# Performance work log

Measured on AMD Instinct MI355X. Metric: run time of the kernel, lower is better.

The kernel has to match this reference:

```python
import jax, jax.numpy as jnp
import numpy as np

N_SPECIES = 119
N_RADIAL = 5
N_BASIS = 7
R_MIN = 0.5
R_MAX = 6.0
UNITS = (512, 512)
EMB_NORM = 1.0 / np.sqrt(N_BASIS)
N_ATOMS = 20000
N_PAIRS = 800000
N_FEAT = 360  # gaussian moments for n_radial=5, n_contr=8

# triangular index sets for symmetric contractions
_t2i, _t2j = np.tril_indices(N_RADIAL)  # 15 unique (r,s) pairs
_t3 = np.array([(i, j, k) for i in range(N_RADIAL) for j in range(i + 1) for k in range(j + 1)])
_t3i, _t3j, _t3k = _t3[:, 0], _t3[:, 1], _t3[:, 2]  # 35 unique (r,s,t) triples


def _forward(R, Z, neighbor, offsets, embeddings, W1, b1, W2, b2, W3, b3):
    n_atoms = R.shape[0]
    idx_i, idx_j = neighbor[0], neighbor[1]
    # --- distance computation (free space, init_box == 0) ---
    dr_vec = R[idx_j] - R[idx_i] + offsets                      # (P,3)
    dr = jnp.sqrt(jnp.sum(dr_vec * dr_vec, axis=-1))            # (P,)
    dn = dr_vec / (dr + 1e-5)[:, None]                          # unit vectors
    # --- gaussian radial basis + species-pair embedding + cosine cutoff ---
    shifts = jnp.linspace(R_MIN, R_MAX, N_BASIS)
    betta = N_BASIS ** 2 / R_MAX ** 2
    rad_norm = (2.0 * betta / np.pi) ** 0.75
    basis = rad_norm * jnp.exp(-betta * (dr[:, None] - shifts) ** 2)   # (P,B)
    cutoff = 0.5 * (jnp.cos(np.pi * dr / R_MAX) + 1.0) * (dr < R_MAX)
    emb = embeddings[Z[idx_j], Z[idx_i]]                               # (P,R,B)
    radial = EMB_NORM * jnp.einsum('prb,pb->pr', emb, basis) * cutoff[:, None]  # (P,R)
    # --- geometric moments, aggregated per central atom ---
    m1 = radial[:, :, None] * dn[:, None, :]                    # (P,R,3)
    m2 = m1[..., None] * dn[:, None, None, :]                   # (P,R,3,3)
    m3 = m2[..., None] * dn[:, None, None, None, :]             # (P,R,3,3,3)
    seg = lambda x: jax.ops.segment_sum(x, idx_i, num_segments=n_atoms)
    M0, M1, M2, M3 = seg(radial), seg(m1), seg(m2), seg(m3)
    # --- invariant contractions (gaussian moments) ---
    c1 = jnp.einsum('ari,asi->ars', M1, M1)[:, _t2i, _t2j]
    c2 = jnp.einsum('arij,asij->ars', M2, M2)[:, _t2i, _t2j]
    c3 = jnp.einsum('arijk,asijk->ars', M3, M3)[:, _t2i, _t2j]
    c4 = jnp.einsum('arij,asik,atjk->arst', M2, M2, M2)[:, _t3i, _t3j, _t3k]
    c5 = jnp.einsum('ari,asj,atij->arst', M1, M1, M2)[:, _t2i, _t2j].reshape(n_atoms, -1)
    c6 = jnp.einsum('arijk,asijl,atkl->arst', M3, M3, M2)[:, _t2i, _t2j].reshape(n_atoms, -1)
    c7 = jnp.einsum('arijk,asij,atk->arst', M3, M2, M1).reshape(n_atoms, -1)
    feats = jnp.concatenate([M0, c1, c2, c3, c4, c5, c6, c7], axis=-1)  # (A,360)
    # --- vmapped per-atom NTK readout MLP (swish) ---
    h = jax.nn.swish(feats @ W1 / np.sqrt(N_FEAT) + 0.1 * b1)
    h = jax.nn.swish(h @ W2 / np.sqrt(UNITS[0]) + 0.1 * b2)
    out = h @ W3 / np.sqrt(UNITS[1]) + 0.1 * b3                 # (A,1)
    # --- mask padded atoms (Z == 0) ---
    out = out * (Z > 0)[:, None]
    return out


def setup_inputs() -> dict:
    key = jax.random.key(0)
    ks = jax.random.split(key, 8)
    R = jax.random.uniform(ks[0], (N_ATOMS, 3), jnp.float32) * 12.0  # 12 A cube
    Z = jax.random.randint(ks[1], (N_ATOMS,), 0, N_SPECIES, jnp.int32)
    neighbor = jax.random.randint(ks[2], (2, N_PAIRS), 0, N_ATOMS, jnp.int32)
    # avoid degenerate self pairs (dr == 0 would NaN the unit vector grad)
    idx_i, idx_j = neighbor[0], neighbor[1]
    idx_j = jnp.where(idx_j == idx_i, (idx_j + 1) % N_ATOMS, idx_j)
    neighbor = jnp.stack([idx_i, idx_j], axis=0)
    box = jnp.zeros((3, 3), jnp.float32)
    offsets = jnp.zeros((N_PAIRS, 3), jnp.float32)
    embeddings = jax.random.normal(ks[3], (N_SPECIES, N_SPECIES, N_RADIAL, N_BASIS), jnp.float32)
    W1 = jax.random.normal(ks[4], (N_FEAT, UNITS[0]), jnp.float32)
    b1 = jnp.zeros((UNITS[0],), jnp.float32)
    W2 = jax.random.normal(ks[5], (UNITS[0], UNITS[1]), jnp.float32)
    b2 = jnp.zeros((UNITS[1],), jnp.float32)
    W3 = jax.random.normal(ks[6], (UNITS[1], 1), jnp.float32)
    b3 = jnp.zeros((1,), jnp.float32)
    return dict(R=R, Z=Z, neighbor=neighbor, box=box, offsets=offsets,
                embeddings=embeddings, W1=W1, b1=b1, W2=W2, b2=b2, W3=W3, b3=b3)


def reference(R, Z, neighbor, box, offsets, embeddings, W1, b1, W2, b2, W3, b3):
    # box is unused: init_box == 0 selects the free-space displacement fn
    return _forward(R, Z, neighbor, offsets, embeddings, W1, b1, W2, b2, W3, b3)
```

## Files before the change

### kernel.cpp

```cpp
#include <hip/hip_runtime.h>
#include <hip/hip_bf16.h>
#include <cmath>

#define NSP 119
#define UNITS 512
#define NFEAT 360
#define KP1 384
#define CAP 128

typedef __attribute__((ext_vector_type(8))) short short8;
typedef __attribute__((ext_vector_type(4))) float floatx4;

#define AS1 __attribute__((address_space(1)))
#define AS3 __attribute__((address_space(3)))

__device__ __forceinline__ void gload_lds16(const void* g, void* l) {
    __builtin_amdgcn_global_load_lds((AS1 void*)(size_t)g, (AS3 void*)l, 16, 0, 0);
}

__device__ __host__ constexpr int s2c(int i, int j) {
    return (i > j) ? i*(i+1)/2 + j : j*(j+1)/2 + i;
}
__device__ __host__ constexpr int s3c(int x, int y, int z) {
    int A = x > y ? x : y; A = A > z ? A : z;
    int C = x < y ? x : y; C = C < z ? C : z;
    int B = x + y + z - A - C;
    return A*(A+1)*(A+2)/6 + B*(B+1)/2 + C;
}

struct BasisConsts {
    float f0k;
    float kg;
    float scale;
    float c[6];
};

__global__ __launch_bounds__(256) void pair_prep_kernel(
    const float* __restrict__ R, const int* __restrict__ Z,
    const int* __restrict__ nbr, const float* __restrict__ offsets,
    const float* __restrict__ emb, int* __restrict__ counts,
    float* __restrict__ tmpRec, int npairs, BasisConsts bc,
    const float* __restrict__ W1, const float* __restrict__ W2,
    __hip_bfloat16* __restrict__ W1t, __hip_bfloat16* __restrict__ W2t,
    float* __restrict__ outbuf, const float* __restrict__ b3,
    int pgrid, int natoms)
{
    int blk = blockIdx.x;
    if (blk >= pgrid) {
        int b = blk - pgrid;
        if (b < 448) {
            __shared__ float tile[32][33];
            const float* W; __hip_bfloat16* Wt; int K, Kp, ik, in;
            if (b < 192) { W = W1; Wt = W1t; K = NFEAT; Kp = KP1; ik = b % 12; in = b / 12; }
            else { int b2 = b - 192; W = W2; Wt = W2t; K = UNITS; Kp = UNITS; ik = b2 & 15; in = b2 >> 4; }
            int tx = threadIdx.x & 31, ty = threadIdx.x >> 5;
            int n = in * 32 + tx;
            #pragma unroll
            for (int pp = 0; pp < 4; ++pp) {
                int kk = ty + pp * 8;
                int k = ik * 32 + kk;
                tile[kk][tx] = (k < K) ? W[(size_t)k * UNITS + n] : 0.f;
            }
            __syncthreads();
            #pragma unroll
            for (int pp = 0; pp < 4; ++pp) {
                int nn = ty + pp * 8;
                Wt[(size_t)(in * 32 + nn) * Kp + ik * 32 + tx] = __float2bfloat16(tile[tx][nn]);
            }
        } else {
            int idx = (b - 448) * 256 + threadIdx.x;
            if (idx < natoms)
                outbuf[idx] = (Z[idx] > 0) ? 0.1f * b3[0] : 0.f;
        }
        return;
    }

    int p = blk * 256 + threadIdx.x;
    if (p >= npairs) return;
    int i = nbr[p];
    int j = nbr[npairs + p];
    float dx = R[3*j]   - R[3*i]   + offsets[3*p];
    float dy = R[3*j+1] - R[3*i+1] + offsets[3*p+1];
    float dz = R[3*j+2] - R[3*i+2] + offsets[3*p+2];
    float dr2 = fmaf(dz, dz, fmaf(dy, dy, dx*dx));
    if (dr2 >= 36.0f) return;
    int pos = atomicAdd(&counts[i], 1);
    if (pos >= CAP) return;

    float dr  = sqrtf(dr2);
    float inv = 1.0f / (dr + 1e-5f);
    float d0  = dr - 0.5f;
    float basis[7];
    basis[0] = exp2f(bc.f0k * d0 * d0);
    float G  = exp2f(bc.kg * dr);
    float cur = basis[0];
    #pragma unroll
    for (int b = 0; b < 6; ++b) { cur *= G * bc.c[b]; basis[b+1] = cur; }
    float cut = 0.5f * (__cosf(dr * 0.52359877559829887f) + 1.0f);
    float s = bc.scale * cut;

    const float* e = emb + ((size_t)Z[j] * NSP + Z[i]) * 35;
    float ev[35];
    __builtin_memcpy(ev, e, 35 * sizeof(float));

    float rec[8];
    #pragma unroll
    for (int r = 0; r < 5; ++r) {
        float acc = 0.f;
        #pragma unroll
        for (int b = 0; b < 7; ++b) acc += ev[r*7+b] * basis[b];
        rec[r] = s * acc;
    }
    rec[5] = dx * inv; rec[6] = dy * inv; rec[7] = dz * inv;
    float4* out = (float4*)(tmpRec + ((size_t)i * CAP + pos) * 8);
    out[0] = make_float4(rec[0], rec[1], rec[2], rec[3]);
    out[1] = make_float4(rec[4], rec[5], rec[6], rec[7]);
}

#define SREC 28
__global__ __launch_bounds__(256) void moment_kernel(
    const float* __restrict__ tmpRec, const int* __restrict__ counts,
    float* __restrict__ momG, int natoms)
{
    int wv = threadIdx.x >> 6, lane = threadIdx.x & 63;
    int a = blockIdx.x * 4 + wv;
    __shared__ float stage[4][64][SREC];

    int cnt = 0;
    if (a < natoms) cnt = min(counts[a], CAP);

    int cr0, pk0;
    if (lane < 5)       { cr0 = lane;            pk0 = 0; }
    else if (lane < 20) { int c = lane - 5;      cr0 = c / 3;  pk0 = 1 + c % 3; }
    else if (lane < 50) { int c = lane - 20;     cr0 = c / 6;  pk0 = 4 + c % 6; }
    else                { int c = lane - 50;     cr0 = c / 10; pk0 = 10 + c % 10; }
    int cr1 = 0, pk1 = 0;
    if (lane < 36) { int c = 14 + lane; cr1 = c / 10; pk1 = 10 + c % 10; }

    float acc0 = 0.f, acc1 = 0.f;
    for (int base = 0; base < cnt; base += 64) {
        int m = min(64, cnt - base);
        if (lane < m) {
            const float4* pd = (const float4*)(tmpRec + ((size_t)a * CAP + base + lane) * 8);
            float4 u = pd[0], v = pd[1];
            float x = v.y, y = v.z, z = v.w;
            float s2_0 = x*x, s2_1 = y*x, s2_2 = y*y, s2_3 = z*x, s2_4 = z*y, s2_5 = z*z;
            float* st = stage[wv][lane];
            ((float4*)st)[0] = u;
            ((float4*)st)[1] = make_float4(v.x, 1.0f, x, y);
            ((float4*)st)[2] = make_float4(z, s2_0, s2_1, s2_2);
            ((float4*)st)[3] = make_float4(s2_3, s2_4, s2_5, s2_0*x);
            ((float4*)st)[4] = make_float4(s2_0*y, s2_2*x, s2_2*y, s2_0*z);
            ((float4*)st)[5] = make_float4(s2_1*z, s2_2*z, s2_5*x, s2_5*y);
            ((float4*)st)[6] = make_float4(s2_5*z, 0.f, 0.f, 0.f);
        }
        __builtin_amdgcn_wave_barrier();
        for (int q = 0; q < m; ++q) {
            const float* s = stage[wv][q];
            acc0 += s[cr0] * s[5 + pk0];
            acc1 += s[cr1] * s[5 + pk1];
        }
        __builtin_amdgcn_wave_barrier();
    }
    size_t base = (size_t)(a >> 6) * 6400 + (size_t)(a & 63);
    momG[base + (size_t)lane * 64] = acc0;
    if (lane < 36) momG[base + (size_t)(64 + lane) * 64] = acc1;
}

#define LROW 390
__global__ __launch_bounds__(256) void feat_kernel(
    const float* __restrict__ momG, __hip_bfloat16* __restrict__ feats)
{
    constexpr int cT2I[15] = {0,1,1,2,2,2,3,3,3,3,4,4,4,4,4};
    constexpr int cT2J[15] = {0,0,1,0,1,2,0,1,2,3,0,1,2,3,4};
    constexpr int cT3A[35] = {0, 1,1,1, 2,2,2,2,2,2, 3,3,3,3,3,3,3,3,3,3, 4,4,4,4,4,4,4,4,4,4,4,4,4,4,4};
    constexpr int cT3B[35] = {0, 0,1,1, 0,1,1,2,2,2, 0,1,1,2,2,2,3,3,3,3, 0,1,1,2,2,2,3,3,3,3,4,4,4,4,4};
    constexpr int cT3C[35] = {0, 0,0,1, 0,0,1,0,1,2, 0,0,1,0,1,2,0,1,2,3, 0,0,1,0,1,2,0,1,2,3,0,1,2,3,4};
    constexpr float cW2[6]  = {1.f,2.f,1.f,2.f,2.f,1.f};
    constexpr float cW3[10] = {1.f,3.f,3.f,1.f,3.f,6.f,3.f,3.f,3.f,1.f};

    __shared__ __hip_bfloat16 ldsF[64][LROW];
    int wv = threadIdx.x >> 6, lane = threadIdx.x & 63;
    const float* mg = momG + (size_t)blockIdx.x * 6400 + lane;

    #define LDM(e) mg[(e) * 64]
    #define STF(f, v) ldsF[lane][(f)] = __float2bfloat16(v)

    if (wv == 0) {
        float m3[50], m2[30];
        #pragma unroll
        for (int e = 0; e < 50; ++e) m3[e] = LDM(50 + e);
        #pragma unroll
        for (int e = 0; e < 30; ++e) m2[e] = LDM(20 + e);
        #pragma unroll
        for (int p = 0; p < 10; ++p) {
            int r = cT2I[p], s = cT2J[p];
            float B2v[9];
            #pragma unroll
            for (int z = 0; z < 3; ++z)
                #pragma unroll
                for (int w = 0; w < 3; ++w) {
                    float acc = 0.f;
                    #pragma unroll
                    for (int x = 0; x < 3; ++x)
                        #pragma unroll
                        for (int y = 0; y < 3; ++y)
                            acc += m3[r*10 + s3c(x,y,z)] * m3[s*10 + s3c(x,y,w)];
                    B2v[z*3+w] = acc;
                }
            #pragma unroll
            for (int t = 0; t < 5; ++t) {
                float acc = 0.f;
                #pragma unroll
                for (int z = 0; z < 3; ++z)
                    #pragma unroll
                    for (int w = 0; w < 3; ++w)
                        acc += B2v[z*3+w] * m2[t*6 + s2c(z,w)];
                STF(160 + p*5 + t, acc);
            }
        }
    } else if (wv == 1) {
        float m0[5], m1[15], m2[30];
        #pragma unroll
        for (int e = 0; e < 5; ++e)  m0[e] = LDM(e);
        #pragma unroll
        for (int e = 0; e < 15; ++e) m1[e] = LDM(5 + e);
        #pragma unroll
        for (int e = 0; e < 30; ++e) m2[e] = LDM(20 + e);
        #pragma unroll
        for (int r = 0; r < 5; ++r) STF(r, m0[r]);
        #pragma unroll
        for (int p = 0; p < 15; ++p) {
            int r = cT2I[p], s = cT2J[p];
            float v1 = m1[r*3]*m1[s*3] + m1[r*3+1]*m1[s*3+1] + m1[r*3+2]*m1[s*3+2];
            STF(5 + p, v1);
            float v2 = 0.f;
            #pragma unroll
            for (int k = 0; k < 6; ++k) v2 += cW2[k] * m2[r*6+k] * m2[s*6+k];
            STF(20 + p, v2);
        }
        #pragma unroll
        for (int q = 0; q < 35; ++q) {
            int r = cT3A[q], s = cT3B[q], t = cT3C[q];
            float v = 0.f;
            #pragma unroll
            for (int x = 0; x < 3; ++x)
                #pragma unroll
                for (int y = 0; y < 3; ++y) {
                    float d = 0.f;
                    #pragma unroll
                    for (int z = 0; z < 3; ++z)
                        d += m2[s*6 + s2c(x,z)] * m2[t*6 + s2c(y,z)];
                    v += m2[r*6 + s2c(x,y)] * d;
                }
            STF(50 + q, v);
        }
        #pragma unroll
        for (int f = NFEAT; f < KP1; ++f) STF(f, 0.f);
    } else if (wv == 2) {
        float m1[15], m2[30], m3[50];
        #pragma unroll
        for (int e = 0; e < 15; ++e) m1[e] = LDM(5 + e);
        #pragma unroll
        for (int e = 0; e < 30; ++e) m2[e] = LDM(20 + e);
        #pragma unroll
        for (int e = 0; e < 50; ++e) m3[e] = LDM(50 + e);
        #pragma unroll
        for (int p = 10; p < 15; ++p) {
            int r = cT2I[p], s = cT2J[p];
            float B2v[9];
            #pragma unroll
            for (int z = 0; z < 3; ++z)
                #pragma unroll
                for (int w = 0; w < 3; ++w) {
                    float acc = 0.f;
                    #pragma unroll
                    for (int x = 0; x < 3; ++x)
                        #pragma unroll
                        for (int y = 0; y < 3; ++y)
                            acc += m3[r*10 + s3c(x,y,z)] * m3[s*10 + s3c(x,y,w)];
                    B2v[z*3+w] = acc;
                }
            #pragma unroll
            for (int t = 0; t < 5; ++t) {
                float acc = 0.f;
                #pragma unroll
                for (int z = 0; z < 3; ++z)
                    #pragma unroll
                    for (int w = 0; w < 3; ++w)
                        acc += B2v[z*3+w] * m2[t*6 + s2c(z,w)];
                STF(160 + p*5 + t, acc);
            }
        }
        #pragma unroll
        for (int p = 0; p < 15; ++p) {
            int r = cT2I[p], s = cT2J[p];
            float o[9];
            #pragma unroll
            for (int x = 0; x < 3; ++x)
                #pragma unroll
                for (int y = 0; y < 3; ++y) o[x*3+y] = m1[r*3+x] * m1[s*3+y];
            #pragma unroll
            for (int t = 0; t < 5; ++t) {
                float v = 0.f;
                #pragma unroll
                for (int x = 0; x < 3; ++x)
                    #pragma unroll
                    for (int y = 0; y < 3; ++y)
                        v += o[x*3+y] * m2[t*6 + s2c(x,y)];
                STF(85 + p*5 + t, v);
            }
        }
    } else {
        float m1[15], m2[30], m3[50];
        #pragma unroll
        for (int e = 0; e < 15; ++e) m1[e] = LDM(5 + e);
        #pragma unroll
        for (int e = 0; e < 30; ++e) m2[e] = LDM(20 + e);
        #pragma unroll
        for (int e = 0; e < 50; ++e) m3[e] = LDM(50 + e);
        #pragma unroll
        for (int p = 0; p < 15; ++p) {
            int r = cT2I[p], s = cT2J[p];
            float v = 0.f;
            #pragma unroll
            for (int k = 0; k < 10; ++k) v += cW3[k] * m3[r*10+k] * m3[s*10+k];
            STF(35 + p, v);
        }
        #pragma unroll
        for (int r = 0; r < 5; ++r)
            #pragma unroll
            for (int s = 0; s < 5; ++s) {
                float A3z[3];
                #pragma unroll
                for (int z = 0; z < 3; ++z) {
                    float v = 0.f;
                    #pragma unroll
                    for (int x = 0; x < 3; ++x)
                        #pragma unroll
                        for (int y = 0; y < 3; ++y)
                            v += m3[r*10 + s3c(x,y,z)] * m2[s*6 + s2c(x,y)];
                    A3z[z] = v;
                }
                #pragma unroll
                for (int t = 0; t < 5; ++t) {
                    float v = A3z[0]*m1[t*3] + A3z[1]*m1[t*3+1] + A3z[2]*m1[t*3+2];
                    STF(235 + r*25 + s*5 + t, v);
                }
            }
    }
    __syncthreads();

    __hip_bfloat16* dst = feats + (size_t)blockIdx.x * 64 * KP1;
    #pragma unroll
    for (int rr = 0; rr < 16; ++rr) {
        int row = wv * 16 + rr;
        #pragma unroll
        for (int it = 0; it < 3; ++it) {
            uint32_t v = *(const uint32_t*)&ldsF[row][(it*64 + lane)*2];
            *(uint32_t*)&dst[(size_t)row * KP1 + (size_t)(it*64 + lane)*2] = v;
        }
    }
    #undef LDM
    #undef STF
}

__global__ __launch_bounds__(256) void gemm_mfma_swish(
    const __hip_bfloat16* __restrict__ A, const __hip_bfloat16* __restrict__ Bt,
    const float* __restrict__ bias, __hip_bfloat16* __restrict__ C,
    const float* __restrict__ w3, float* __restrict__ outacc,
    const int* __restrict__ Zmask,
    int Kp, int M, int Mtiles, float alpha, float a3, int fuse)
{
    __shared__ float4 As[2][512];
    __shared__ float4 Bs[2][512];
    int tid = threadIdx.x;
    int wave = tid >> 6, lane = tid & 63;
    int quad = lane >> 4, l16 = lane & 15;
    int wm = wave >> 1, wn = wave & 1;
    int bid = blockIdx.x;
    int mt = (bid >> 5) * 8 + (bid & 7);
    int nt = (bid >> 3) & 3;
    if (mt >= Mtiles) return;
    int rowBase = mt * 128;
    int colBase = nt * 128;

    floatx4 acc[4][4] = {};

    int r0 = tid >> 2, c0 = (tid & 3) ^ ((r0 >> 1) & 3);
    int r1 = r0 + 64,  c1 = (tid & 3) ^ ((r1 >> 1) & 3);

    const char* gA0 = (const char*)A  + ((size_t)(rowBase + r0) * Kp) * 2 + c0 * 16;
    const char* gA1 = (const char*)A  + ((size_t)(rowBase + r1) * Kp) * 2 + c1 * 16;
    const char* gB0 = (const char*)Bt + ((size_t)(colBase + r0) * Kp) * 2 + c0 * 16;
    const char* gB1 = (const char*)Bt + ((size_t)(colBase + r1) * Kp) * 2 + c1 * 16;

    char* lA = (char*)As;
    char* lB = (char*)Bs;
    int wvoff = wave << 10;

    int posA[4], posB[4];
    #pragma unroll
    for (int t = 0; t < 4; ++t) {
        int rr = wm * 64 + t * 16 + l16;
        posA[t] = rr * 4 + (quad ^ ((rr >> 1) & 3));
    }
    #pragma unroll
    for (int u = 0; u < 4; ++u) {
        int cc = wn * 64 + u * 16 + l16;
        posB[u] = cc * 4 + (quad ^ ((cc >> 1) & 3));
    }

    int nK = Kp >> 5;

    {
        int lo = wvoff;
        gload_lds16(gA0, lA + lo);
        gload_lds16(gA1, lA + lo + 4096);
        gload_lds16(gB0, lB + lo);
        gload_lds16(gB1, lB + lo + 4096);
    }
    __syncthreads();

    for (int kt = 0; kt < nK; ++kt) {
        int buf = kt & 1;
        if (kt + 1 < nK) {
            int go = (kt + 1) << 6;
            int lo = ((buf ^ 1) << 13) + wvoff;
            gload_lds16(gA0 + go, lA + lo);
            gload_lds16(gA1 + go, lA + lo + 4096);
            gload_lds16(gB0 + go, lB + lo);
            gload_lds16(gB1 + go, lB + lo + 4096);
        }
        short8 af[4], bf[4];
        #pragma unroll
        for (int t = 0; t < 4; ++t) af[t] = *(const short8*)(As[buf] + posA[t]);
        #pragma unroll
        for (int u = 0; u < 4; ++u) bf[u] = *(const short8*)(Bs[buf] + posB[u]);
        #pragma unroll
        for (int t = 0; t < 4; ++t)
            #pragma unroll
            for (int u = 0; u < 4; ++u)
                acc[t][u] = __builtin_amdgcn_mfma_f32_16x16x32_bf16(
                    af[t], bf[u], acc[t][u], 0, 0, 0);
        __syncthreads();
    }

    if (!fuse) {
        #pragma unroll
        for (int u = 0; u < 4; ++u) {
            int col = colBase + wn * 64 + u * 16 + l16;
            float bc = 0.1f * bias[col];
            #pragma unroll
            for (int t = 0; t < 4; ++t) {
                int row0 = rowBase + wm * 64 + t * 16 + quad * 4;
                #pragma unroll
                for (int r = 0; r < 4; ++r) {
                    float x = alpha * acc[t][u][r] + bc;
                    float v = x / (1.f + expf(-x));
                    C[(size_t)(row0 + r) * UNITS + col] = __float2bfloat16(v);
                }
            }
        }
    } else {
        float rowsum[4][4] = {};
        #pragma unroll
        for (int u = 0; u < 4; ++u) {
            int col = colBase + wn * 64 + u * 16 + l16;
            float bc = 0.1f * bias[col];
            float w3c = w3[col] * a3;
            #pragma unroll
            for (int t = 0; t < 4; ++t)
                #pragma unroll
                for (int r = 0; r < 4; ++r) {
                    float x = alpha * acc[t][u][r] + bc;
                    float v = x / (1.f + expf(-x));
                    rowsum[t][r] += v * w3c;
                }
        }
        #pragma unroll
        for (int t = 0; t < 4; ++t)
            #pragma unroll
            for (int r = 0; r < 4; ++r) {
                float s = rowsum[t][r];
                s += __shfl_xor(s, 1, 64);
                s += __shfl_xor(s, 2, 64);
                s += __shfl_xor(s, 4, 64);
                s += __shfl_xor(s, 8, 64);
                rowsum[t][r] = s;
            }
        if (l16 == 0) {
            #pragma unroll
            for (int t = 0; t < 4; ++t) {
                int row0 = rowBase + wm * 64 + t * 16 + quad * 4;
                #pragma unroll
                for (int r = 0; r < 4; ++r) {
                    int row = row0 + r;
                    if (row < M && Zmask[row] > 0)
                        atomicAdd(&outacc[row], rowsum[t][r]);
                }
            }
        }
    }
}

static inline size_t align_up(size_t x, size_t a) { return (x + a - 1) & ~(a - 1); }

extern "C" void kernel_launch(void* const* d_in, const int* in_sizes, int n_in,
                              void* d_out, int out_size, void* d_ws, size_t ws_size,
                              hipStream_t stream)
{
    const float* R       = (const float*)d_in[0];
    const int*   Z       = (const int*)  d_in[1];
    const int*   nbr     = (const int*)  d_in[2];
    const float* offsets = (const float*)d_in[4];
    const float* emb     = (const float*)d_in[5];
    const float* W1      = (const float*)d_in[6];
    const float* b1      = (const float*)d_in[7];
    const float* W2      = (const float*)d_in[8];
    const float* b2      = (const float*)d_in[9];
    const float* W3      = (const float*)d_in[10];
    const float* b3      = (const float*)d_in[11];

    int natoms = in_sizes[0] / 3;
    int npairs = in_sizes[2] / 2;
    int Mpad = ((natoms + 127) / 128) * 128;
    int Mtiles = Mpad / 128;

    char* ws = (char*)d_ws;
    size_t off = 0;
    int* counts = (int*)(ws + off); off = align_up(off + natoms*4, 256);
    float* tmpRec = (float*)(ws + off); off = align_up(off + (size_t)natoms*CAP*8*4, 256);
    float* momG = (float*)(ws + off); off = align_up(off + (size_t)Mpad*100*4, 256);
    __hip_bfloat16* W1t   = (__hip_bfloat16*)(ws + off); off = align_up(off + (size_t)UNITS*KP1*2, 256);
    __hip_bfloat16* W2t   = (__hip_bfloat16*)(ws + off); off = align_up(off + (size_t)UNITS*UNITS*2, 256);
    __hip_bfloat16* feats = (__hip_bfloat16*)(ws + off); off = align_up(off + (size_t)Mpad*KP1*2, 256);
    __hip_bfloat16* h1    = (__hip_bfloat16*)(ws + off); off = align_up(off + (size_t)Mpad*UNITS*2, 256);

    BasisConsts bc;
    {
        const double betta = 49.0 / 36.0;
        const double delta = 5.5 / 6.0;
        const double log2e = 1.4426950408889634073599246810;
        bc.f0k = (float)(-betta * log2e);
        bc.kg  = (float)(2.0 * betta * delta * log2e);
        for (int b = 0; b < 6; ++b)
            bc.c[b] = (float)exp(-betta * delta * (1.0 + delta * (2*b + 1)));
        bc.scale = (float)(pow(2.0 * betta / M_PI, 0.75) / sqrt(7.0));
    }

    hipMemsetAsync(counts, 0, (size_t)natoms * sizeof(int), stream);

    int pgrid = (npairs + 255) / 256;
    int totalBlocks = pgrid + 448 + (natoms + 255) / 256;
    pair_prep_kernel<<<dim3(totalBlocks), 256, 0, stream>>>(
        R, Z, nbr, offsets, emb, counts, tmpRec, npairs, bc,
        W1, W2, W1t, W2t, (float*)d_out, b3, pgrid, natoms);

    moment_kernel<<<dim3(Mpad / 4), 256, 0, stream>>>(
        tmpRec, counts, momG, natoms);
    feat_kernel<<<dim3(Mpad / 64), 256, 0, stream>>>(momG, feats);

    float a1 = 1.0f / sqrtf((float)NFEAT);
    float a2 = 1.0f / sqrtf((float)UNITS);
    int gemmGrid = ((Mtiles + 7) / 8) * 8 * 4;
    gemm_mfma_swish<<<dim3(gemmGrid), 256, 0, stream>>>(
        feats, W1t, b1, h1, nullptr, nullptr, nullptr, KP1, natoms, Mtiles, a1, 0.f, 0);
    gemm_mfma_swish<<<dim3(gemmGrid), 256, 0, stream>>>(
        h1, W2t, b2, nullptr, W3, (float*)d_out, Z, UNITS, natoms, Mtiles, a2, a2, 1);
}
```

Measured before the change: 200.4 us.

## Triple-buffer GEMM K-loop with explicit vmcnt waits and single barrier

New measurement: 205.0 us. 2.3% more time.

```diff
diff --git a/kernel.cpp b/kernel.cpp
--- a/kernel.cpp
+++ b/kernel.cpp
@@ -372,8 +372,8 @@
     const int* __restrict__ Zmask,
     int Kp, int M, int Mtiles, float alpha, float a3, int fuse)
 {
-    __shared__ float4 As[2][512];
-    __shared__ float4 Bs[2][512];
+    __shared__ float4 As[3][512];
+    __shared__ float4 Bs[3][512];
     int tid = threadIdx.x;
     int wave = tid >> 6, lane = tid & 63;
     int quad = lane >> 4, l16 = lane & 15;
@@ -413,38 +413,35 @@
 
     int nK = Kp >> 5;
 
-    {
-        int lo = wvoff;
-        gload_lds16(gA0, lA + lo);
-        gload_lds16(gA1, lA + lo + 4096);
-        gload_lds16(gB0, lB + lo);
-        gload_lds16(gB1, lB + lo + 4096);
-    }
-    __syncthreads();
+    #define STAGE(b, kt) { int go_ = (kt) << 6; int lo_ = ((b) << 13) + wvoff;  \
+        gload_lds16(gA0 + go_, lA + lo_);                                       \
+        gload_lds16(gA1 + go_, lA + lo_ + 4096);                                \
+        gload_lds16(gB0 + go_, lB + lo_);                                       \
+        gload_lds16(gB1 + go_, lB + lo_ + 4096); }
+
+    STAGE(0, 0);
+    STAGE(1, 1);
 
     for (int kt = 0; kt < nK; ++kt) {
-        int buf = kt & 1;
-        if (kt + 1 < nK) {
-            int go = (kt + 1) << 6;
-            int lo = ((buf ^ 1) << 13) + wvoff;
-            gload_lds16(gA0 + go, lA + lo);
-            gload_lds16(gA1 + go, lA + lo + 4096);
-            gload_lds16(gB0 + go, lB + lo);
-            gload_lds16(gB1 + go, lB + lo + 4096);
-        }
+        int b = kt % 3;
+        if (kt + 1 < nK) asm volatile("s_waitcnt vmcnt(4)" ::: "memory");
+        else             asm volatile("s_waitcnt vmcnt(0)" ::: "memory");
+        __builtin_amdgcn_s_barrier();
+        __builtin_amdgcn_sched_barrier(0);
+        if (kt + 2 < nK) { int b2 = (kt + 2) % 3; STAGE(b2, kt + 2); }
         short8 af[4], bf[4];
         #pragma unroll
-        for (int t = 0; t < 4; ++t) af[t] = *(const short8*)(As[buf] + posA[t]);
-        #pragma unroll
-        for (int u = 0; u < 4; ++u) bf[u] = *(const short8*)(Bs[buf] + posB[u]);
+        for (int t = 0; t < 4; ++t) af[t] = *(const short8*)(As[b] + posA[t]);
+        #pragma unroll
+        for (int u = 0; u < 4; ++u) bf[u] = *(const short8*)(Bs[b] + posB[u]);
         #pragma unroll
         for (int t = 0; t < 4; ++t)
             #pragma unroll
             for (int u = 0; u < 4; ++u)
                 acc[t][u] = __builtin_amdgcn_mfma_f32_16x16x32_bf16(
                     af[t], bf[u], acc[t][u], 0, 0, 0);
-        __syncthreads();
-    }
+    }
+    #undef STAGE
 
     if (!fuse) {
         #pragma unroll
```
